# Performance work log

Measured on AMD Instinct MI355X. Metric: run time of the kernel, lower is better.

## Reference

```python
import jax, jax.numpy as jnp
import numpy as np

V = 778   # MANO mesh vertex count (hard-coded in the module)
K = 9     # spiral neighborhood length
C = 256   # in_channels
OUT = 3   # out_channels (per-vertex offset xyz)
B3 = 192  # 3 * B, B = 64


def setup_inputs() -> dict:
    key = jax.random.key(0)
    ks = jax.random.split(key, 12)
    x = jax.random.normal(ks[0], (B3, V, C), jnp.float32)
    pred_occ = jax.random.normal(ks[1], (B3, 2, 5), jnp.float32)
    indices = jax.random.randint(ks[2], (V, K), 0, V)
    finger_sizes = [112, 120, 124, 116, 108]
    fingers = {f"finger{i}": jax.random.randint(ks[3 + i], (n,), 0, V)
               for i, n in enumerate(finger_sizes)}

    def lin(k, fan_in, fan_out):
        kw, kb = jax.random.split(k)
        w = jax.random.normal(kw, (fan_in, fan_out), jnp.float32) / np.float32(np.sqrt(fan_in))
        b = jax.random.normal(kb, (fan_out,), jnp.float32) * 0.01
        return w, b

    w0, b0 = lin(ks[8], 2 * C * K, 2 * C)
    w1, b1 = lin(ks[9], 2 * C * K, C)
    w2, b2 = lin(ks[10], C * K, C)
    wh, bh = lin(ks[11], C * K, OUT)
    return {"x": x, "pred_occ": pred_occ, "indices": indices, **fingers,
            "w0": w0, "b0": b0, "w1": w1, "b1": b1, "w2": w2, "b2": b2,
            "wh": wh, "bh": bh}


def spiral_conv(x, idx, w, b):
    # x: [B, V, Cin], idx: [V, K] -> gather spiral neighbors, flatten, linear
    B = x.shape[0]
    g = x[:, idx.reshape(-1), :].reshape(B, V, -1)  # [B, V, K*Cin]
    return g @ w + b


def reference(x, pred_occ, indices, finger0, finger1, finger2, finger3, finger4,
              w0, b0, w1, b1, w2, b2, wh, bh):
    # Per-finger non-occlusion probabilities: softmax over class dim, take class 0
    occ = jax.nn.softmax(pred_occ, axis=1)[:, 0, :5]          # [3B, 5]
    weights = jnp.ones((x.shape[0], V), x.dtype)
    for i, fidx in enumerate([finger0, finger1, finger2, finger3, finger4]):
        val = jnp.broadcast_to(occ[:, i:i + 1], (x.shape[0], fidx.shape[0]))
        weights = weights.at[:, fidx].set(val)
    B = x.shape[0] // 3
    wv = jnp.stack(jnp.split(weights, 3, axis=0), axis=-1)[..., None]  # [B, V, 3, 1]
    wv = jax.nn.softmax(wv, axis=2)
    xv = jnp.stack(jnp.split(x, 3, axis=0), axis=2)                    # [B, V, 3, C]
    wx = jnp.sum(wv * xv, axis=2)                                      # [B, V, C]
    h = jnp.concatenate([wx, x[:B]], axis=2)                           # [B, V, 2C]
    h = jax.nn.relu(spiral_conv(h, indices, w0, b0))
    h = jax.nn.relu(spiral_conv(h, indices, w1, b1))
    h = jax.nn.relu(spiral_conv(h, indices, w2, b2))
    return spiral_conv(h, indices, wh, bh)                             # [B, V, 3]
```

## Files before the change

kernel.cpp:

```cpp
#include <hip/hip_runtime.h>

typedef unsigned short ushort_t;
typedef __attribute__((ext_vector_type(8))) __bf16 bf16x8;
typedef __attribute__((ext_vector_type(8))) unsigned short ushort8;
typedef __attribute__((ext_vector_type(4))) float floatx4;
typedef __attribute__((ext_vector_type(16))) float floatx16;

#define VN 778
#define KNB 9

__device__ __forceinline__ float bf2f(unsigned short s) {
  union { unsigned int u; float f; } x; x.u = ((unsigned int)s) << 16; return x.f;
}
__device__ __forceinline__ unsigned short f2bf(float f) {
  union { float f; unsigned int u; } x; x.f = f;
  unsigned int r = x.u + 0x7fffu + ((x.u >> 16) & 1u);
  return (unsigned short)(r >> 16);
}

__device__ __forceinline__ void load_lds16(const void* g, void* l) {
  __builtin_amdgcn_global_load_lds(
      (const __attribute__((address_space(1))) unsigned int*)g,
      (__attribute__((address_space(3))) unsigned int*)l, 16, 0, 0);
}

__device__ __forceinline__ int xcd_swizzle(int g, int nwg) {
  int q = nwg >> 3, r = nwg & 7;
  int xcd = g & 7, o = g >> 3;
  return (xcd < r ? xcd * (q + 1) : r * (q + 1) + (xcd - r) * q) + o;
}

__global__ void prep_misc(const float* __restrict__ pred_occ,
                          const int* f0, const int* f1, const int* f2,
                          const int* f3, const int* f4,
                          int n0, int n1, int n2, int n3, int n4,
                          const float* __restrict__ wh,
                          float* __restrict__ occ, int* __restrict__ fid,
                          float* __restrict__ whT) {
  int t = threadIdx.x;
  for (int i = t; i < 192 * 5; i += 256) {
    int r = i / 5, f = i % 5;
    float p0 = pred_occ[r * 10 + f];
    float p1 = pred_occ[r * 10 + 5 + f];
    occ[i] = 1.0f / (1.0f + __expf(p1 - p0));
  }
  for (int i = t; i < VN; i += 256) fid[i] = -1;
  __syncthreads();
  const int* fp[5] = {f0, f1, f2, f3, f4};
  int fn[5] = {n0, n1, n2, n3, n4};
  for (int fi = 0; fi < 5; ++fi) {
    for (int i = t; i < fn[fi]; i += 256) fid[fp[fi][i]] = fi;
    __syncthreads();
  }
  for (int i = t; i < 3 * 2304; i += 256) {
    int o = i / 2304, k = i % 2304;
    whT[i] = wh[k * 3 + o];
  }
}

__global__ void wx_kernel(const float* __restrict__ x, const float* __restrict__ occ,
                          const int* __restrict__ fid, ushort_t* __restrict__ wx) {
  int g = blockIdx.x * 256 + threadIdx.x;
  int c8 = (g & 31) << 3;
  int bv = g >> 5;
  int b = bv / VN;
  int v = bv - b * VN;
  int f = fid[v];
  float w0 = 1.f, w1 = 1.f, w2 = 1.f;
  if (f >= 0) {
    w0 = occ[b * 5 + f];
    w1 = occ[(64 + b) * 5 + f];
    w2 = occ[(128 + b) * 5 + f];
  }
  float m = fmaxf(w0, fmaxf(w1, w2));
  float e0 = __expf(w0 - m), e1 = __expf(w1 - m), e2 = __expf(w2 - m);
  float inv = 1.0f / (e0 + e1 + e2);
  e0 *= inv; e1 *= inv; e2 *= inv;
  size_t base = (size_t)bv * 256 + c8;
  const size_t V1 = (size_t)64 * VN * 256, V2 = (size_t)128 * VN * 256;
  floatx4 x0a = *(const floatx4*)(x + base);
  floatx4 x0b = *(const floatx4*)(x + base + 4);
  floatx4 x1a = *(const floatx4*)(x + V1 + base);
  floatx4 x1b = *(const floatx4*)(x + V1 + base + 4);
  floatx4 x2a = *(const floatx4*)(x + V2 + base);
  floatx4 x2b = *(const floatx4*)(x + V2 + base + 4);
  ushort8 o;
#pragma unroll
  for (int e = 0; e < 4; ++e) {
    o[e]     = f2bf(e0 * x0a[e] + e1 * x1a[e] + e2 * x2a[e]);
    o[e + 4] = f2bf(e0 * x0b[e] + e1 * x1b[e] + e2 * x2b[e]);
  }
  *(ushort8*)(wx + base) = o;
}

__global__ void xcvt_kernel(const float* __restrict__ x, ushort_t* __restrict__ xb) {
  int g = blockIdx.x * 256 + threadIdx.x;
  size_t base = (size_t)g * 8;
  floatx4 fa = *(const floatx4*)(x + base);
  floatx4 fb = *(const floatx4*)(x + base + 4);
  ushort8 o;
#pragma unroll
  for (int e = 0; e < 4; ++e) { o[e] = f2bf(fa[e]); o[e + 4] = f2bf(fb[e]); }
  *(ushort8*)(xb + base) = o;
}

__global__ void pack_w(const float* __restrict__ w, ushort_t* __restrict__ wP,
                       int N, int ksn, int total) {
  int chunk = blockIdx.x * 256 + threadIdx.x;
  if (chunk >= total) return;
  int lane = chunk & 63;
  int rest = chunk >> 6;
  int ks = rest % ksn;
  int tn = rest / ksn;
  int n = (tn << 5) + (lane & 31);
  int kb = (ks << 4) + ((lane >> 5) << 3);
  ushort8 o;
#pragma unroll
  for (int j = 0; j < 8; ++j) o[j] = f2bf(w[(size_t)(kb + j) * N + n]);
  *(ushort8*)(wP + (size_t)chunk * 8) = o;
}

template <int CIN, int MODE>
__global__ __launch_bounds__(512, 4) void spiral_gemm(
    const ushort_t* __restrict__ act0, const float* __restrict__ actF,
    const ushort_t* __restrict__ actB, const ushort_t* __restrict__ wP,
    const float* __restrict__ bias, const int* __restrict__ idx,
    ushort_t* __restrict__ out, int NOUT, int nbx) {
  constexpr int H = CIN / 128;
  constexpr int P = KNB * H;
  __shared__ __align__(16) ushort_t Alds[2][2048 * 8];
  const int wgid = xcd_swizzle(blockIdx.x, gridDim.x);
  const int yb = wgid / nbx;
  const int xb = wgid - yb * nbx;
  const int v0 = xb * 2;
  const int n0 = yb << 8;
  const int tid = threadIdx.x;
  const int lane = tid & 63;
  const int wv = tid >> 6;
  const int mlo = lane & 31;
  const int q = lane >> 5;
  const int xm = mlo & 7;
  floatx16 acc0{}, acc1{}, acc2{}, acc3{};
  const int KtotSteps = KNB * (CIN / 16);
  const int tn0 = (n0 >> 5) + wv;
  const ushort_t* bp = wP + (size_t)tn0 * KtotSteps * 512 + lane * 8;
  const int* iv0 = idx + v0 * KNB;
  const int* iv1 = iv0 + KNB;
  const int aoff0 = mlo * 128;
  const int aoff1 = (mlo + 32) * 128;
  const int aoff2 = 8192 + mlo * 128;
  const int aoff3 = 8192 + (mlo + 32) * 128;

  auto dma_stage = [&](int p, ushort_t* buf) {
    const int nbr = p / H, h = p - nbr * H;
    const int nva = iv0[nbr], nvb = iv1[nbr];
#pragma unroll
    for (int it = 0; it < 4; ++it) {
      const int slotb = ((wv << 2) + it) << 6;
      const int s = slotb + lane;
      const int vv = s >> 10;
      const int row = (s >> 4) & 63;
      const int ck = (s & 15) ^ (row & 7);
      const int nv = vv ? nvb : nva;
      const ushort_t* src;
      if (MODE == 0) {
        src = act0 + ((size_t)(row * VN + nv)) * CIN + h * 128 + ck * 8;
      } else {
        const ushort_t* basep = (MODE == 1 || h < 2) ? act0 : actB;
        src = basep + ((size_t)(row * VN + nv)) * 256 + (h & 1) * 128 + ck * 8;
      }
      load_lds16(src, buf + (size_t)slotb * 8);
    }
  };
  auto f32_stage = [&](int p, ushort_t* buf) {
    const int nbr = p / H, h = p - nbr * H;
    const int nva = iv0[nbr], nvb = iv1[nbr];
#pragma unroll
    for (int j = 0; j < 4; ++j) {
      const int s = (j << 9) + tid;
      const int vv = s >> 10;
      const int row = (s >> 4) & 63;
      const int ck = (s & 15) ^ (row & 7);
      const int nv = vv ? nvb : nva;
      const float* src = actF + ((size_t)(row * VN + nv)) * 256 + (h - 2) * 128 + ck * 8;
      floatx4 fa = *(const floatx4*)src;
      floatx4 fb = *(const floatx4*)(src + 4);
      ushort8 o;
#pragma unroll
      for (int e = 0; e < 4; ++e) { o[e] = f2bf(fa[e]); o[e + 4] = f2bf(fb[e]); }
      *(ushort8*)(buf + (size_t)s * 8) = o;
    }
  };

  dma_stage(0, Alds[0]);
  __syncthreads();
#pragma unroll 2
  for (int p = 0; p < P; ++p) {
    ushort_t* cur = Alds[p & 1];
    ushort_t* nxt = Alds[(p + 1) & 1];
    const bool have_next = (p + 1 < P);
    const bool next_f32 = (MODE == 1) && (((p + 1) & (H - 1)) >= 2);
    if (have_next && !next_f32) dma_stage(p + 1, nxt);
#pragma unroll
    for (int ks = 0; ks < 8; ++ks) {
      const int cko = ((((ks << 1) + q) ^ xm) << 3);
      bf16x8 a0 = *(const bf16x8*)(cur + aoff0 + cko);
      bf16x8 a1 = *(const bf16x8*)(cur + aoff1 + cko);
      bf16x8 a2 = *(const bf16x8*)(cur + aoff2 + cko);
      bf16x8 a3 = *(const bf16x8*)(cur + aoff3 + cko);
      bf16x8 bv = *(const bf16x8*)bp; bp += 512;
      acc0 = __builtin_amdgcn_mfma_f32_32x32x16_bf16(a0, bv, acc0, 0, 0, 0);
      acc1 = __builtin_amdgcn_mfma_f32_32x32x16_bf16(a1, bv, acc1, 0, 0, 0);
      acc2 = __builtin_amdgcn_mfma_f32_32x32x16_bf16(a2, bv, acc2, 0, 0, 0);
      acc3 = __builtin_amdgcn_mfma_f32_32x32x16_bf16(a3, bv, acc3, 0, 0, 0);
    }
    __syncthreads();
    if (have_next && next_f32) { f32_stage(p + 1, nxt); __syncthreads(); }
  }
  const int n = n0 + (wv << 5) + mlo;
  const float bn = bias[n];
#pragma unroll
  for (int t = 0; t < 4; ++t) {
    const floatx16 av = (t == 0) ? acc0 : (t == 1) ? acc1 : (t == 2) ? acc2 : acc3;
    const int vcur = v0 + (t >> 1);
    const int bbase = (t & 1) << 5;
#pragma unroll
    for (int r = 0; r < 16; ++r) {
      const int m = (r & 3) + ((r >> 2) << 3) + (q << 2);
      float val = av[r] + bn; val = val > 0.f ? val : 0.f;
      out[((size_t)((bbase + m) * VN + vcur)) * NOUT + n] = f2bf(val);
    }
  }
}

__global__ void head_kernel(const ushort_t* __restrict__ act, const float* __restrict__ whT,
                            const float* __restrict__ bh, const int* __restrict__ idx,
                            float* __restrict__ out) {
  __shared__ __align__(16) ushort_t Alds[64 * 256];
  const int v = xcd_swizzle(blockIdx.x, gridDim.x);
  const int tid = threadIdx.x;
  float a0 = 0.f, a1 = 0.f, a2 = 0.f;
  const int b = tid;
  const int xm = b & 7;
  for (int nbr = 0; nbr < KNB; ++nbr) {
    const int nv = idx[v * KNB + nbr];
    __syncthreads();
#pragma unroll
    for (int it = 0; it < 8; ++it) {
      int L = it * 256 + tid;
      int bb = L >> 5;
      int jj = L & 31;
      ushort8 val = *(const ushort8*)(act + ((size_t)(bb * VN + nv)) * 256 + (jj << 3));
      int slot = jj ^ (bb & 7);
      *(ushort8*)&Alds[(size_t)(bb * 32 + slot) * 8] = val;
    }
    __syncthreads();
    if (tid < 64) {
      const float* wp = whT + nbr * 256;
#pragma unroll 4
      for (int j = 0; j < 32; ++j) {
        int jj = j ^ xm;
        ushort8 a8 = *(const ushort8*)&Alds[(b * 32 + jj) * 8];
#pragma unroll
        for (int e = 0; e < 8; ++e) {
          float av = bf2f(a8[e]);
          int k = (j << 3) + e;
          a0 += av * wp[k];
          a1 += av * wp[2304 + k];
          a2 += av * wp[4608 + k];
        }
      }
    }
  }
  if (tid < 64) {
    size_t o = ((size_t)(b * VN + v)) * 3;
    out[o + 0] = a0 + bh[0];
    out[o + 1] = a1 + bh[1];
    out[o + 2] = a2 + bh[2];
  }
}

extern "C" void kernel_launch(void* const* d_in, const int* in_sizes, int n_in,
                              void* d_out, int out_size, void* d_ws, size_t ws_size,
                              hipStream_t stream) {
  const float* x        = (const float*)d_in[0];
  const float* pred_occ = (const float*)d_in[1];
  const int* indices    = (const int*)d_in[2];
  const int* f0 = (const int*)d_in[3];
  const int* f1 = (const int*)d_in[4];
  const int* f2 = (const int*)d_in[5];
  const int* f3 = (const int*)d_in[6];
  const int* f4 = (const int*)d_in[7];
  const float* w0 = (const float*)d_in[8];
  const float* b0 = (const float*)d_in[9];
  const float* w1 = (const float*)d_in[10];
  const float* b1 = (const float*)d_in[11];
  const float* w2 = (const float*)d_in[12];
  const float* b2 = (const float*)d_in[13];
  const float* wh = (const float*)d_in[14];
  const float* bh = (const float*)d_in[15];
  float* outp = (float*)d_out;

  char* ws = (char*)d_ws;
  ushort_t* wP0 = (ushort_t*)(ws + 0);
  ushort_t* wP1 = (ushort_t*)(ws + 4718592);
  ushort_t* wP2 = (ushort_t*)(ws + 7077888);
  float* whT    = (float*)(ws + 8257536);
  float* occ    = (float*)(ws + 8285184);
  int* fid      = (int*)(ws + 8289024);
  ushort_t* R0  = (ushort_t*)(ws + 8292352);
  ushort_t* R1  = (ushort_t*)(ws + 33785856);
  ushort_t* XB  = (ushort_t*)(ws + 84772864);
  const bool useXB = (ws_size >= 110266368ull);

  prep_misc<<<1, 256, 0, stream>>>(pred_occ, f0, f1, f2, f3, f4,
                                   in_sizes[3], in_sizes[4], in_sizes[5],
                                   in_sizes[6], in_sizes[7], wh, occ, fid, whT);
  pack_w<<<294912 / 256, 256, 0, stream>>>(w0, wP0, 512, 288, 294912);
  pack_w<<<147456 / 256, 256, 0, stream>>>(w1, wP1, 256, 288, 147456);
  pack_w<<<73728 / 256, 256, 0, stream>>>(w2, wP2, 256, 144, 73728);
  if (useXB) xcvt_kernel<<<6224, 256, 0, stream>>>(x, XB);
  wx_kernel<<<6224, 256, 0, stream>>>(x, occ, fid, R0);

  if (useXB)
    spiral_gemm<512, 2><<<778, 512, 0, stream>>>(R0, nullptr, XB, wP0, b0,
                                                 indices, R1, 512, 389);
  else
    spiral_gemm<512, 1><<<778, 512, 0, stream>>>(R0, x, nullptr, wP0, b0,
                                                 indices, R1, 512, 389);
  spiral_gemm<512, 0><<<389, 512, 0, stream>>>(R1, nullptr, nullptr, wP1, b1,
                                               indices, R0, 256, 389);
  spiral_gemm<256, 0><<<389, 512, 0, stream>>>(R0, nullptr, nullptr, wP2, b2,
                                               indices, R1, 256, 389);
  head_kernel<<<VN, 256, 0, stream>>>(R1, whT, bh, indices, outp);
  (void)n_in; (void)out_size;
}
```

Before: 812.3 us.

## Use per-vertex 256-thread spiral GEMM with 64-wide N tiles for layers 1-2

Adds a new spiral GEMM kernel for the second and third conv layers. Each workgroup handles one vertex and all 64 batch rows. Each of its four waves computes a 64x64 output tile from four 32x32x16 MFMAs per k-step, reading weights straight from global memory in a new 64-column packed layout. This replaces the 389-block, 512-thread launches with 778 smaller blocks, aiming for better occupancy and more reuse of weight fragments. The trade-off is more weight traffic per block, since every block streams the full weight matrix.

```diff
diff --git a/kernel.cpp b/kernel.cpp
--- a/kernel.cpp
+++ b/kernel.cpp
@@ -113,6 +113,24 @@
   int ks = rest % ksn;
   int tn = rest / ksn;
   int n = (tn << 5) + (lane & 31);
+  int kb = (ks << 4) + ((lane >> 5) << 3);
+  ushort8 o;
+#pragma unroll
+  for (int j = 0; j < 8; ++j) o[j] = f2bf(w[(size_t)(kb + j) * N + n]);
+  *(ushort8*)(wP + (size_t)chunk * 8) = o;
+}
+
+__global__ void pack_w64(const float* __restrict__ w, ushort_t* __restrict__ wP,
+                         int N, int ksn, int total) {
+  int chunk = blockIdx.x * 256 + threadIdx.x;
+  if (chunk >= total) return;
+  int lane = chunk & 63;
+  int idx2 = chunk >> 6;
+  int sub = idx2 & 1;
+  int rest = idx2 >> 1;
+  int ks = rest % ksn;
+  int tn64 = rest / ksn;
+  int n = (tn64 << 6) + (sub << 5) + (lane & 31);
   int kb = (ks << 4) + ((lane >> 5) << 3);
   ushort8 o;
 #pragma unroll
@@ -233,6 +251,82 @@
   }
 }
 
+template <int CIN>
+__global__ __launch_bounds__(256, 4) void spiral_gemm_v1(
+    const ushort_t* __restrict__ act, const ushort_t* __restrict__ wP,
+    const float* __restrict__ bias, const int* __restrict__ idx,
+    ushort_t* __restrict__ out) {
+  constexpr int H = CIN / 128;
+  constexpr int P = KNB * H;
+  constexpr int KtotSteps = KNB * (CIN / 16);
+  __shared__ __align__(16) ushort_t Alds[2][1024 * 8];
+  const int v = xcd_swizzle(blockIdx.x, gridDim.x);
+  const int tid = threadIdx.x;
+  const int lane = tid & 63;
+  const int wv = tid >> 6;
+  const int mlo = lane & 31;
+  const int q = lane >> 5;
+  const int xm = mlo & 7;
+  floatx16 c00{}, c01{}, c10{}, c11{};
+  const ushort_t* bp = wP + (size_t)wv * KtotSteps * 1024 + lane * 8;
+  const int* iv = idx + v * KNB;
+  const int aoff0 = mlo * 128;
+  const int aoff1 = (mlo + 32) * 128;
+
+  auto dma_stage = [&](int p, ushort_t* buf) {
+    const int nbr = p / H, h = p - nbr * H;
+    const int nv = iv[nbr];
+#pragma unroll
+    for (int it = 0; it < 4; ++it) {
+      const int slotb = ((wv << 2) + it) << 6;
+      const int s = slotb + lane;
+      const int row = (s >> 4) & 63;
+      const int ck = (s & 15) ^ (row & 7);
+      const ushort_t* src = act + ((size_t)(row * VN + nv)) * CIN + h * 128 + ck * 8;
+      load_lds16(src, buf + (size_t)slotb * 8);
+    }
+  };
+
+  dma_stage(0, Alds[0]);
+  __syncthreads();
+#pragma unroll 2
+  for (int p = 0; p < P; ++p) {
+    ushort_t* cur = Alds[p & 1];
+    if (p + 1 < P) dma_stage(p + 1, Alds[(p + 1) & 1]);
+#pragma unroll
+    for (int ks = 0; ks < 8; ++ks) {
+      const int cko = ((((ks << 1) + q) ^ xm) << 3);
+      bf16x8 a0 = *(const bf16x8*)(cur + aoff0 + cko);
+      bf16x8 a1 = *(const bf16x8*)(cur + aoff1 + cko);
+      bf16x8 b0 = *(const bf16x8*)bp;
+      bf16x8 b1 = *(const bf16x8*)(bp + 512);
+      bp += 1024;
+      c00 = __builtin_amdgcn_mfma_f32_32x32x16_bf16(a0, b0, c00, 0, 0, 0);
+      c10 = __builtin_amdgcn_mfma_f32_32x32x16_bf16(a1, b0, c10, 0, 0, 0);
+      c01 = __builtin_amdgcn_mfma_f32_32x32x16_bf16(a0, b1, c01, 0, 0, 0);
+      c11 = __builtin_amdgcn_mfma_f32_32x32x16_bf16(a1, b1, c11, 0, 0, 0);
+    }
+    __syncthreads();
+  }
+  const int nb = (wv << 6) + mlo;
+  const float bn0 = bias[nb];
+  const float bn1 = bias[nb + 32];
+#pragma unroll
+  for (int t = 0; t < 4; ++t) {
+    const int mi = t >> 1;
+    const int ni = t & 1;
+    const floatx16 av = (t == 0) ? c00 : (t == 1) ? c01 : (t == 2) ? c10 : c11;
+    const int n = nb + (ni << 5);
+    const float bn = ni ? bn1 : bn0;
+#pragma unroll
+    for (int r = 0; r < 16; ++r) {
+      const int m = (r & 3) + ((r >> 2) << 3) + (q << 2) + (mi << 5);
+      float val = av[r] + bn; val = val > 0.f ? val : 0.f;
+      out[((size_t)(m * VN + v)) * 256 + n] = f2bf(val);
+    }
+  }
+}
+
 __global__ void head_kernel(const ushort_t* __restrict__ act, const float* __restrict__ whT,
                             const float* __restrict__ bh, const int* __restrict__ idx,
                             float* __restrict__ out) {
@@ -317,8 +411,8 @@
                                    in_sizes[3], in_sizes[4], in_sizes[5],
                                    in_sizes[6], in_sizes[7], wh, occ, fid, whT);
   pack_w<<<294912 / 256, 256, 0, stream>>>(w0, wP0, 512, 288, 294912);
-  pack_w<<<147456 / 256, 256, 0, stream>>>(w1, wP1, 256, 288, 147456);
-  pack_w<<<73728 / 256, 256, 0, stream>>>(w2, wP2, 256, 144, 73728);
+  pack_w64<<<147456 / 256, 256, 0, stream>>>(w1, wP1, 256, 288, 147456);
+  pack_w64<<<73728 / 256, 256, 0, stream>>>(w2, wP2, 256, 144, 73728);
   if (useXB) xcvt_kernel<<<6224, 256, 0, stream>>>(x, XB);
   wx_kernel<<<6224, 256, 0, stream>>>(x, occ, fid, R0);
 
@@ -328,10 +422,8 @@
   else
     spiral_gemm<512, 1><<<778, 512, 0, stream>>>(R0, x, nullptr, wP0, b0,
                                                  indices, R1, 512, 389);
-  spiral_gemm<512, 0><<<389, 512, 0, stream>>>(R1, nullptr, nullptr, wP1, b1,
-                                               indices, R0, 256, 389);
-  spiral_gemm<256, 0><<<389, 512, 0, stream>>>(R0, nullptr, nullptr, wP2, b2,
-                                               indices, R1, 256, 389);
+  spiral_gemm_v1<512><<<778, 256, 0, stream>>>(R1, wP1, b1, indices, R0);
+  spiral_gemm_v1<256><<<778, 256, 0, stream>>>(R0, wP2, b2, indices, R1);
   head_kernel<<<VN, 256, 0, stream>>>(R1, whT, bh, indices, outp);
   (void)n_in; (void)out_size;
 }
```

New measurement: 914.3 us. +12.6%, slower.
